# Optimization experiments

Measured on AMD Instinct MI355X. Metric: run time of the kernel, lower is better.

The kernel has to match this reference:

```python
import jax, jax.numpy as jnp
import numpy as np

N, C_IN, C_OUT = 16384, 512, 1024

def setup_inputs() -> dict:
    key = jax.random.key(0)
    k1, k2 = jax.random.split(key)
    x = jax.random.normal(k1, (N, C_IN), dtype=jnp.float32)
    mean = jax.random.normal(k2, (C_OUT, C_IN), dtype=jnp.float32)
    return {"x": x, "mean": mean}

def reference(x, mean):
    # out[n, o] = 1 / sqrt(sum_c (x[n,c] - mean[o,c])^2)
    x_sq = jnp.sum(x * x, axis=-1, keepdims=True)            # [N, 1]
    m_sq = jnp.sum(mean * mean, axis=-1)                     # [O]
    cross = jnp.einsum('nc,oc->no', x, mean)                 # [N, O] GEMM
    d2 = x_sq - 2.0 * cross + m_sq[None, :]                  # [N, O]
    return jax.lax.rsqrt(d2)
```

## Files before the change

kernel.cpp:

```cpp
#include <hip/hip_runtime.h>
#include <hip/hip_bf16.h>
#include <stdint.h>

#define N_ROWS 16384
#define O_ROWS 1024
#define K_DIM  512

typedef __bf16 bf16x8 __attribute__((ext_vector_type(8)));
typedef float  f32x4  __attribute__((ext_vector_type(4)));

__device__ __forceinline__ ushort f2bfu(float f) {
    __bf16 h = (__bf16)f;
    return __builtin_bit_cast(ushort, h);
}

#define BAR_LGKM()  do {                                        \
    asm volatile("s_waitcnt lgkmcnt(0)" ::: "memory");          \
    __builtin_amdgcn_s_barrier();                               \
} while (0)

__global__ __launch_bounds__(512) void quadra_kernel(
    const float* __restrict__ x, const float* __restrict__ mean,
    float* __restrict__ out)
{
    __shared__ ushort sA[256 * 64];
    __shared__ ushort sB[128 * 64];

    const int bid  = blockIdx.x;
    const int t    = (bid & 7) * 64 + (bid >> 3);
    const int brow = (t >> 3) * 256;
    const int bcol = (t & 7) * 128;

    const int tid  = threadIdx.x;
    const int lane = tid & 63;
    const int wid  = tid >> 6;
    const int wr = wid >> 1, wc = wid & 1;

    f32x4 acc[4][4] = {};

    const int r0 = tid >> 3;
    const int q  = tid & 7;

    const float* gA = x    + (size_t)(brow + r0) * K_DIM + q * 8;
    const float* gB = mean + (size_t)(bcol + r0) * K_DIM + q * 8;

    float asq[4] = {0.f, 0.f, 0.f, 0.f};
    float bsq[2] = {0.f, 0.f};

    const int hi = lane >> 4, cl = lane & 15;

    #pragma unroll 1
    for (int kt = 0; kt < 8; ++kt) {
        #pragma unroll
        for (int i = 0; i < 4; ++i) {
            const float* p = gA + (size_t)(i * 64) * K_DIM + kt * 64;
            f32x4 v0 = *(const f32x4*)(p);
            f32x4 v1 = *(const f32x4*)(p + 4);

            asq[i] += v0[0]*v0[0] + v0[1]*v0[1] + v0[2]*v0[2] + v0[3]*v0[3]
                    + v1[0]*v1[0] + v1[1]*v1[1] + v1[2]*v1[2] + v1[3]*v1[3];

            bf16x8 cv;
            cv[0] = (__bf16)v0[0]; cv[1] = (__bf16)v0[1];
            cv[2] = (__bf16)v0[2]; cv[3] = (__bf16)v0[3];
            cv[4] = (__bf16)v1[0]; cv[5] = (__bf16)v1[1];
            cv[6] = (__bf16)v1[2]; cv[7] = (__bf16)v1[3];

            const int row = r0 + i * 64;
            const int wb  = (q * 16) ^ ((row & 7) << 4);
            *(bf16x8*)(sA + row * 64 + (wb >> 1)) = cv;
        }
        #pragma unroll
        for (int i = 0; i < 2; ++i) {
            const float* p = gB + (size_t)(i * 64) * K_DIM + kt * 64;
            f32x4 v0 = *(const f32x4*)(p);
            f32x4 v1 = *(const f32x4*)(p + 4);

            bsq[i] += v0[0]*v0[0] + v0[1]*v0[1] + v0[2]*v0[2] + v0[3]*v0[3]
                    + v1[0]*v1[0] + v1[1]*v1[1] + v1[2]*v1[2] + v1[3]*v1[3];

            bf16x8 cv;
            cv[0] = (__bf16)(v0[0] * -2.0f); cv[1] = (__bf16)(v0[1] * -2.0f);
            cv[2] = (__bf16)(v0[2] * -2.0f); cv[3] = (__bf16)(v0[3] * -2.0f);
            cv[4] = (__bf16)(v1[0] * -2.0f); cv[5] = (__bf16)(v1[1] * -2.0f);
            cv[6] = (__bf16)(v1[2] * -2.0f); cv[7] = (__bf16)(v1[3] * -2.0f);

            const int row = r0 + i * 64;
            const int wb  = (q * 16) ^ ((row & 7) << 4);
            *(bf16x8*)(sB + row * 64 + (wb >> 1)) = cv;
        }

        BAR_LGKM();

        #pragma unroll
        for (int ks = 0; ks < 2; ++ks) {
            bf16x8 a[4], b[4];
            #pragma unroll
            for (int m = 0; m < 4; ++m) {
                const int row = wr*64 + m*16 + cl;
                const int rb  = (ks*64 + hi*16) ^ ((row & 7) << 4);
                a[m] = *(const bf16x8*)(sA + row * 64 + (rb >> 1));
            }
            #pragma unroll
            for (int n = 0; n < 4; ++n) {
                const int row = wc*64 + n*16 + cl;
                const int rb  = (ks*64 + hi*16) ^ ((row & 7) << 4);
                b[n] = *(const bf16x8*)(sB + row * 64 + (rb >> 1));
            }
            #pragma unroll
            for (int m = 0; m < 4; ++m)
                #pragma unroll
                for (int n = 0; n < 4; ++n)
                    acc[m][n] = __builtin_amdgcn_mfma_f32_16x16x32_bf16(
                        a[m], b[n], acc[m][n], 0, 0, 0);
        }

        BAR_LGKM();
    }

    ushort* sAe = sA;
    ushort* sBe = sA + 256 * 32;
    #pragma unroll
    for (int i = 0; i < 4; ++i) {
        float sa = asq[i];
        #pragma unroll
        for (int msk = 1; msk < 8; msk <<= 1) sa += __shfl_xor(sa, msk);
        uint2 aw = {0u, 0u};
        if (q == 0) aw.x = (uint32_t)f2bfu(sa) | (0x3F80u << 16);
        *(uint2*)(sAe + (r0 + i * 64) * 32 + q * 4) = aw;
    }
    #pragma unroll
    for (int i = 0; i < 2; ++i) {
        float sb = bsq[i];
        #pragma unroll
        for (int msk = 1; msk < 8; msk <<= 1) sb += __shfl_xor(sb, msk);
        uint2 bw = {0u, 0u};
        if (q == 0) bw.x = 0x3F80u | ((uint32_t)f2bfu(sb) << 16);
        *(uint2*)(sBe + (r0 + i * 64) * 32 + q * 4) = bw;
    }
    BAR_LGKM();

    {
        bf16x8 a[4], b[4];
        #pragma unroll
        for (int m = 0; m < 4; ++m)
            a[m] = *(const bf16x8*)(sAe + (wr*64 + m*16 + cl) * 32 + hi * 8);
        #pragma unroll
        for (int n = 0; n < 4; ++n)
            b[n] = *(const bf16x8*)(sBe + (wc*64 + n*16 + cl) * 32 + hi * 8);
        #pragma unroll
        for (int m = 0; m < 4; ++m)
            #pragma unroll
            for (int n = 0; n < 4; ++n)
                acc[m][n] = __builtin_amdgcn_mfma_f32_16x16x32_bf16(
                    a[m], b[n], acc[m][n], 0, 0, 0);
    }

    const int rg = lane >> 4;
    #pragma unroll
    for (int m = 0; m < 4; ++m) {
        #pragma unroll
        for (int j = 0; j < 4; ++j) {
            const int grow = brow + wr*64 + m*16 + rg*4 + j;
            float* orow = out + (size_t)grow * O_ROWS + bcol + wc*64 + cl;
            #pragma unroll
            for (int n = 0; n < 4; ++n)
                orow[n * 16] = rsqrtf(acc[m][n][j]);
        }
    }
}

extern "C" void kernel_launch(void* const* d_in, const int* in_sizes, int n_in,
                              void* d_out, int out_size, void* d_ws, size_t ws_size,
                              hipStream_t stream) {
    const float* x    = (const float*)d_in[0];
    const float* mean = (const float*)d_in[1];
    float* out = (float*)d_out;

    quadra_kernel<<<dim3((N_ROWS / 256) * (O_ROWS / 128)), 512, 0, stream>>>(
        x, mean, out);
}
```

Baseline: 40.59 us.

## Double-buffer LDS K-tiles and prefetch next tile into registers during MFMA

The K loop now uses two LDS buffers with a K-tile of 32 instead of 64. Global loads for the next tile are issued before the current tile's MFMAs, and the next buffer is converted and written between the two halves of the MFMA work, so there is one barrier per iteration instead of two. The aim is to hide global load latency and barrier stalls behind matrix math. In exchange the loop runs twice as many iterations with smaller tiles, the staging layout is more complex, and prefetch registers may raise register pressure.

Measured after the change: 48.79 us. +20.2%, slower.

```diff
diff --git a/kernel.cpp b/kernel.cpp
--- a/kernel.cpp
+++ b/kernel.cpp
@@ -23,8 +23,8 @@
     const float* __restrict__ x, const float* __restrict__ mean,
     float* __restrict__ out)
 {
-    __shared__ ushort sA[256 * 64];
-    __shared__ ushort sB[128 * 64];
+    __shared__ ushort sA[2][128 * 64];
+    __shared__ ushort sB[2][64 * 64];
 
     const int bid  = blockIdx.x;
     const int t    = (bid & 7) * 64 + (bid >> 3);
@@ -35,108 +35,132 @@
     const int lane = tid & 63;
     const int wid  = tid >> 6;
     const int wr = wid >> 1, wc = wid & 1;
+    const int cl = lane & 15, hi = lane >> 4;
 
     f32x4 acc[4][4] = {};
 
-    const int r0 = tid >> 3;
-    const int q  = tid & 7;
-
-    const float* gA = x    + (size_t)(brow + r0) * K_DIM + q * 8;
-    const float* gB = mean + (size_t)(bcol + r0) * K_DIM + q * 8;
-
-    float asq[4] = {0.f, 0.f, 0.f, 0.f};
-    float bsq[2] = {0.f, 0.f};
-
-    const int hi = lane >> 4, cl = lane & 15;
+    const int sr    = tid >> 3;
+    const int u2    = tid & 7;
+    const int upair = u2 >> 2;
+    const int uk    = u2 & 3;
+
+    const float* gA = x + (size_t)(brow + sr + upair * 128) * K_DIM + uk * 8;
+    const float* gB = mean + (size_t)(bcol + sr + upair * 64) * K_DIM + uk * 8;
+
+    const int swzA = (sr & 7) << 4;
+    const int offA0 = (sr)      * 64 + (((u2 * 16) ^ swzA) >> 1);
+    const int offA1 = (sr + 64) * 64 + (((u2 * 16) ^ swzA) >> 1);
+    const int offB  = (sr)      * 64 + (((u2 * 16) ^ swzA) >> 1);
+
+    float asq[2] = {0.f, 0.f};
+    float bsq = 0.f;
+
+    f32x4 pa[2][2], pb[2];
+
+    #define LOADK(KT) do {                                                   \
+        pa[0][0] = *(const f32x4*)(gA + (KT) * 32);                          \
+        pa[0][1] = *(const f32x4*)(gA + (KT) * 32 + 4);                      \
+        pa[1][0] = *(const f32x4*)(gA + (size_t)64 * K_DIM + (KT) * 32);     \
+        pa[1][1] = *(const f32x4*)(gA + (size_t)64 * K_DIM + (KT) * 32 + 4); \
+        pb[0]    = *(const f32x4*)(gB + (KT) * 32);                          \
+        pb[1]    = *(const f32x4*)(gB + (KT) * 32 + 4);                      \
+    } while (0)
+
+    #define STAGEK(BUF) do {                                                 \
+        _Pragma("unroll")                                                    \
+        for (int i = 0; i < 2; ++i) {                                        \
+            f32x4 v0 = pa[i][0], v1 = pa[i][1];                              \
+            asq[i] += v0[0]*v0[0] + v0[1]*v0[1] + v0[2]*v0[2] + v0[3]*v0[3]  \
+                    + v1[0]*v1[0] + v1[1]*v1[1] + v1[2]*v1[2] + v1[3]*v1[3]; \
+            bf16x8 cv;                                                       \
+            cv[0] = (__bf16)v0[0]; cv[1] = (__bf16)v0[1];                    \
+            cv[2] = (__bf16)v0[2]; cv[3] = (__bf16)v0[3];                    \
+            cv[4] = (__bf16)v1[0]; cv[5] = (__bf16)v1[1];                    \
+            cv[6] = (__bf16)v1[2]; cv[7] = (__bf16)v1[3];                    \
+            *(bf16x8*)(&sA[BUF][0] + (i ? offA1 : offA0)) = cv;              \
+        }                                                                    \
+        {                                                                    \
+            f32x4 v0 = pb[0], v1 = pb[1];                                    \
+            bsq += v0[0]*v0[0] + v0[1]*v0[1] + v0[2]*v0[2] + v0[3]*v0[3]     \
+                 + v1[0]*v1[0] + v1[1]*v1[1] + v1[2]*v1[2] + v1[3]*v1[3];    \
+            bf16x8 cv;                                                       \
+            cv[0] = (__bf16)(v0[0] * -2.0f); cv[1] = (__bf16)(v0[1] * -2.0f);\
+            cv[2] = (__bf16)(v0[2] * -2.0f); cv[3] = (__bf16)(v0[3] * -2.0f);\
+            cv[4] = (__bf16)(v1[0] * -2.0f); cv[5] = (__bf16)(v1[1] * -2.0f);\
+            cv[6] = (__bf16)(v1[2] * -2.0f); cv[7] = (__bf16)(v1[3] * -2.0f);\
+            *(bf16x8*)(&sB[BUF][0] + offB) = cv;                             \
+        }                                                                    \
+    } while (0)
+
+    LOADK(0);
+    STAGEK(0);
+    BAR_LGKM();
 
     #pragma unroll 1
-    for (int kt = 0; kt < 8; ++kt) {
-        #pragma unroll
-        for (int i = 0; i < 4; ++i) {
-            const float* p = gA + (size_t)(i * 64) * K_DIM + kt * 64;
-            f32x4 v0 = *(const f32x4*)(p);
-            f32x4 v1 = *(const f32x4*)(p + 4);
-
-            asq[i] += v0[0]*v0[0] + v0[1]*v0[1] + v0[2]*v0[2] + v0[3]*v0[3]
-                    + v1[0]*v1[0] + v1[1]*v1[1] + v1[2]*v1[2] + v1[3]*v1[3];
-
-            bf16x8 cv;
-            cv[0] = (__bf16)v0[0]; cv[1] = (__bf16)v0[1];
-            cv[2] = (__bf16)v0[2]; cv[3] = (__bf16)v0[3];
-            cv[4] = (__bf16)v1[0]; cv[5] = (__bf16)v1[1];
-            cv[6] = (__bf16)v1[2]; cv[7] = (__bf16)v1[3];
-
-            const int row = r0 + i * 64;
-            const int wb  = (q * 16) ^ ((row & 7) << 4);
-            *(bf16x8*)(sA + row * 64 + (wb >> 1)) = cv;
-        }
+    for (int kt = 0; kt < 16; ++kt) {
+        const int cur = kt & 1;
+
+        if (kt < 15) LOADK(kt + 1);
+
+        bf16x8 a[4], b[4];
+        #pragma unroll
+        for (int m = 0; m < 4; ++m) {
+            const int row = wr*64 + m*16 + cl;
+            const int lr  = row & 127;
+            const int by  = ((row >> 7) * 64 + hi * 16) ^ ((lr & 7) << 4);
+            a[m] = *(const bf16x8*)(&sA[cur][0] + lr * 64 + (by >> 1));
+        }
+        #pragma unroll
+        for (int n = 0; n < 4; ++n) {
+            const int row = wc*64 + n*16 + cl;
+            const int lr  = row & 63;
+            const int by  = ((row >> 6) * 64 + hi * 16) ^ ((lr & 7) << 4);
+            b[n] = *(const bf16x8*)(&sB[cur][0] + lr * 64 + (by >> 1));
+        }
+
+        #pragma unroll
+        for (int m = 0; m < 2; ++m)
+            #pragma unroll
+            for (int n = 0; n < 4; ++n)
+                acc[m][n] = __builtin_amdgcn_mfma_f32_16x16x32_bf16(
+                    a[m], b[n], acc[m][n], 0, 0, 0);
+
+        if (kt < 15) {
+            if (cur) STAGEK(0); else STAGEK(1);
+        }
+
+        #pragma unroll
+        for (int m = 2; m < 4; ++m)
+            #pragma unroll
+            for (int n = 0; n < 4; ++n)
+                acc[m][n] = __builtin_amdgcn_mfma_f32_16x16x32_bf16(
+                    a[m], b[n], acc[m][n], 0, 0, 0);
+
+        BAR_LGKM();
+    }
+
+    ushort* sAe = &sA[0][0];
+    ushort* sBe = &sA[1][0];
+    {
+        float s0 = asq[0], s1 = asq[1], sb = bsq;
+        s0 += __shfl_xor(s0, 1); s0 += __shfl_xor(s0, 2);
+        s1 += __shfl_xor(s1, 1); s1 += __shfl_xor(s1, 2);
+        sb += __shfl_xor(sb, 1); sb += __shfl_xor(sb, 2);
         #pragma unroll
         for (int i = 0; i < 2; ++i) {
-            const float* p = gB + (size_t)(i * 64) * K_DIM + kt * 64;
-            f32x4 v0 = *(const f32x4*)(p);
-            f32x4 v1 = *(const f32x4*)(p + 4);
-
-            bsq[i] += v0[0]*v0[0] + v0[1]*v0[1] + v0[2]*v0[2] + v0[3]*v0[3]
-                    + v1[0]*v1[0] + v1[1]*v1[1] + v1[2]*v1[2] + v1[3]*v1[3];
-
-            bf16x8 cv;
-            cv[0] = (__bf16)(v0[0] * -2.0f); cv[1] = (__bf16)(v0[1] * -2.0f);
-            cv[2] = (__bf16)(v0[2] * -2.0f); cv[3] = (__bf16)(v0[3] * -2.0f);
-            cv[4] = (__bf16)(v1[0] * -2.0f); cv[5] = (__bf16)(v1[1] * -2.0f);
-            cv[6] = (__bf16)(v1[2] * -2.0f); cv[7] = (__bf16)(v1[3] * -2.0f);
-
-            const int row = r0 + i * 64;
-            const int wb  = (q * 16) ^ ((row & 7) << 4);
-            *(bf16x8*)(sB + row * 64 + (wb >> 1)) = cv;
-        }
-
-        BAR_LGKM();
-
-        #pragma unroll
-        for (int ks = 0; ks < 2; ++ks) {
-            bf16x8 a[4], b[4];
-            #pragma unroll
-            for (int m = 0; m < 4; ++m) {
-                const int row = wr*64 + m*16 + cl;
-                const int rb  = (ks*64 + hi*16) ^ ((row & 7) << 4);
-                a[m] = *(const bf16x8*)(sA + row * 64 + (rb >> 1));
-            }
-            #pragma unroll
-            for (int n = 0; n < 4; ++n) {
-                const int row = wc*64 + n*16 + cl;
-                const int rb  = (ks*64 + hi*16) ^ ((row & 7) << 4);
-                b[n] = *(const bf16x8*)(sB + row * 64 + (rb >> 1));
-            }
-            #pragma unroll
-            for (int m = 0; m < 4; ++m)
-                #pragma unroll
-                for (int n = 0; n < 4; ++n)
-                    acc[m][n] = __builtin_amdgcn_mfma_f32_16x16x32_bf16(
-                        a[m], b[n], acc[m][n], 0, 0, 0);
-        }
-
-        BAR_LGKM();
-    }
-
-    ushort* sAe = sA;
-    ushort* sBe = sA + 256 * 32;
-    #pragma unroll
-    for (int i = 0; i < 4; ++i) {
-        float sa = asq[i];
-        #pragma unroll
-        for (int msk = 1; msk < 8; msk <<= 1) sa += __shfl_xor(sa, msk);
-        uint2 aw = {0u, 0u};
-        if (q == 0) aw.x = (uint32_t)f2bfu(sa) | (0x3F80u << 16);
-        *(uint2*)(sAe + (r0 + i * 64) * 32 + q * 4) = aw;
-    }
-    #pragma unroll
-    for (int i = 0; i < 2; ++i) {
-        float sb = bsq[i];
-        #pragma unroll
-        for (int msk = 1; msk < 8; msk <<= 1) sb += __shfl_xor(sb, msk);
-        uint2 bw = {0u, 0u};
-        if (q == 0) bw.x = 0x3F80u | ((uint32_t)f2bfu(sb) << 16);
-        *(uint2*)(sBe + (r0 + i * 64) * 32 + q * 4) = bw;
+            const int row = sr + i * 64 + upair * 128;
+            uint4 w = {0u, 0u, 0u, 0u};
+            if (uk == 0)
+                w.x = (uint32_t)f2bfu(i ? s1 : s0) | (0x3F80u << 16);
+            *(uint4*)(sAe + row * 32 + uk * 8) = w;
+        }
+        {
+            const int row = sr + upair * 64;
+            uint4 w = {0u, 0u, 0u, 0u};
+            if (uk == 0)
+                w.x = 0x3F80u | ((uint32_t)f2bfu(sb) << 16);
+            *(uint4*)(sBe + row * 32 + uk * 8) = w;
+        }
     }
     BAR_LGKM();
 
@@ -156,18 +180,19 @@
                     a[m], b[n], acc[m][n], 0, 0, 0);
     }
 
-    const int rg = lane >> 4;
     #pragma unroll
     for (int m = 0; m < 4; ++m) {
         #pragma unroll
         for (int j = 0; j < 4; ++j) {
-            const int grow = brow + wr*64 + m*16 + rg*4 + j;
+            const int grow = brow + wr*64 + m*16 + hi*4 + j;
             float* orow = out + (size_t)grow * O_ROWS + bcol + wc*64 + cl;
             #pragma unroll
             for (int n = 0; n < 4; ++n)
                 orow[n * 16] = rsqrtf(acc[m][n][j]);
         }
     }
+    #undef LOADK
+    #undef STAGEK
 }
 
 extern "C" void kernel_launch(void* const* d_in, const int* in_sizes, int n_in,
```
